# Performance work log

Measured on AMD Instinct MI355X. Metric: run time of the kernel, lower is better.

## Reference

```python
import jax, jax.numpy as jnp
import numpy as np

EPS = 1e-16


def setup_inputs() -> dict:
    key = jax.random.key(0)
    k1, k2, k3 = jax.random.split(key, 3)
    nnz, d = 2_000_000, 64
    num_cols = 50_000
    values = jax.random.normal(k1, (nnz, d), dtype=jnp.float32)
    rows = jax.random.randint(k2, (nnz,), 0, num_cols, dtype=jnp.int64)
    cols = jax.random.randint(k3, (nnz,), 0, num_cols, dtype=jnp.int64)
    indices = jnp.stack([rows, cols], axis=0)  # [2, nnz]
    return {"values": values, "indices": indices, "num_cols": num_cols}


def reference(values, indices, num_cols):
    # axis=0: pool over rows -> one pooled vector per column (segment mean),
    # then gather-broadcast back to every nonzero entry.
    seg = indices[1]  # index[1 - axis], the column index of each nnz entry
    # segment sum of values: dense [num_cols, d]
    sums = jax.ops.segment_sum(values, seg, num_segments=num_cols)
    # count of nnz per column (+ eps, matching the torch code)
    cnt = jax.ops.segment_sum(
        jnp.ones(values.shape[0], dtype=values.dtype), seg, num_segments=num_cols
    ) + EPS
    mean = sums / cnt[:, None]  # [num_cols, d]
    return mean[seg]  # [nnz, d]
```

## Files before the change

### kernel.cpp

```cpp
#include <hip/hip_runtime.h>

#define EPS 1e-16f
#define STRIDE 96

typedef float f32x4 __attribute__((ext_vector_type(4)));


__global__ void zero_cnt_kernel(int* __restrict__ ws, const int* __restrict__ nc_p) {
    const int nc = *nc_p;
    for (int i = blockIdx.x * blockDim.x + threadIdx.x; i < nc;
         i += gridDim.x * blockDim.x)
        ws[i] = 0;
}

__global__ void append_kernel(const int* __restrict__ cols, int* __restrict__ ws,
                              const int* __restrict__ nc_p, int nnz) {
    const int nc = *nc_p;
    int* cnt  = ws;
    int* perm = ws + nc;
    const int i = blockIdx.x * blockDim.x + threadIdx.x;
    if (i < nnz) {
        const int c = cols[i];
        const int r = atomicAdd(&cnt[c], 1);
        if (r < STRIDE) perm[c * STRIDE + r] = i;
    }
}

__global__ void pool_kernel(const f32x4* __restrict__ vals4,
                            int* __restrict__ ws,
                            const int* __restrict__ nc_p,
                            f32x4* __restrict__ out4) {
    const int nc = *nc_p;
    const int* cnt  = ws;
    const int* perm = ws + nc;
    const int lane = threadIdx.x & 63;
    const int g  = lane >> 4;
    const int jv = lane & 15;
    const int wave = blockIdx.x * (blockDim.x >> 6) + (threadIdx.x >> 6);
    const int nw = gridDim.x * (blockDim.x >> 6);
    for (int c = wave; c < nc; c += nw) {
        int n = cnt[c];
        if (n == 0) continue;
        n = (n > STRIDE) ? STRIDE : n;
        const int s = c * STRIDE;
        const int e = s + n;
        f32x4 acc = (f32x4)(0.f);
        for (int k = s + g; k < e; k += 4) {
            const int i = perm[k];
            const f32x4 v = __builtin_nontemporal_load(&vals4[(size_t)i * 16 + jv]);
            acc += v;
        }
        #pragma unroll
        for (int off = 16; off < 64; off <<= 1) {
            acc.x += __shfl_xor(acc.x, off);
            acc.y += __shfl_xor(acc.y, off);
            acc.z += __shfl_xor(acc.z, off);
            acc.w += __shfl_xor(acc.w, off);
        }
        const float inv = 1.0f / ((float)n + EPS);
        const f32x4 mean = acc * inv;
        for (int k = s + g; k < e; k += 4) {
            const int i = perm[k];
            __builtin_nontemporal_store(mean, &out4[(size_t)i * 16 + jv]);
        }
    }
}

extern "C" void kernel_launch(void* const* d_in, const int* in_sizes, int n_in,
                              void* d_out, int out_size, void* d_ws, size_t ws_size,
                              hipStream_t stream) {
    const float* values  = (const float*)d_in[0];
    const int*   indices = (const int*)d_in[1];
    const int*   nc_p    = (const int*)d_in[2];

    const int nnz = in_sizes[0] / 64;
    const int* cols = indices + nnz;

    int* ws = (int*)d_ws;

    const int blk = 256;
    const int grid_nnz = (nnz + blk - 1) / blk;

    zero_cnt_kernel<<<64, blk, 0, stream>>>(ws, nc_p);
    append_kernel<<<grid_nnz, blk, 0, stream>>>(cols, ws, nc_p, nnz);
    pool_kernel<<<4096, blk, 0, stream>>>((const f32x4*)values, ws, nc_p,
                                          (f32x4*)d_out);
}
```

Baseline: 409.9 us.

## Fuse zero, append and pool into one persistent kernel with grid barriers

```diff
diff --git a/kernel.cpp b/kernel.cpp
--- a/kernel.cpp
+++ b/kernel.cpp
@@ -6,38 +6,47 @@
 typedef float f32x4 __attribute__((ext_vector_type(4)));
 
 
-__global__ void zero_cnt_kernel(int* __restrict__ ws, const int* __restrict__ nc_p) {
-    const int nc = *nc_p;
-    for (int i = blockIdx.x * blockDim.x + threadIdx.x; i < nc;
-         i += gridDim.x * blockDim.x)
-        ws[i] = 0;
+__device__ __forceinline__ void gbar(int* ctr, int nblk) {
+    __syncthreads();
+    __threadfence();
+    if (threadIdx.x == 0) {
+        __hip_atomic_fetch_add(ctr, 1, __ATOMIC_ACQ_REL, __HIP_MEMORY_SCOPE_AGENT);
+        while (__hip_atomic_load(ctr, __ATOMIC_ACQUIRE, __HIP_MEMORY_SCOPE_AGENT) < nblk)
+            __builtin_amdgcn_s_sleep(4);
+    }
+    __syncthreads();
 }
 
-__global__ void append_kernel(const int* __restrict__ cols, int* __restrict__ ws,
-                              const int* __restrict__ nc_p, int nnz) {
+__global__ __launch_bounds__(256, 8)
+void fused_kernel(const f32x4* __restrict__ vals4,
+                  const int* __restrict__ cols,
+                  const int* __restrict__ nc_p,
+                  f32x4* __restrict__ out4,
+                  int* __restrict__ ws,
+                  int nnz, int nblk) {
     const int nc = *nc_p;
-    int* cnt  = ws;
-    int* perm = ws + nc;
-    const int i = blockIdx.x * blockDim.x + threadIdx.x;
-    if (i < nnz) {
+    int* bars = ws;
+    int* cnt  = ws + 16;
+    int* perm = cnt + nc;
+
+    const int tid = blockIdx.x * blockDim.x + threadIdx.x;
+    const int nth = gridDim.x * blockDim.x;
+
+    for (int i = tid; i < nc; i += nth) cnt[i] = 0;
+    gbar(&bars[0], nblk);
+
+    for (int i = tid; i < nnz; i += nth) {
         const int c = cols[i];
         const int r = atomicAdd(&cnt[c], 1);
         if (r < STRIDE) perm[c * STRIDE + r] = i;
     }
-}
+    gbar(&bars[1], nblk);
 
-__global__ void pool_kernel(const f32x4* __restrict__ vals4,
-                            int* __restrict__ ws,
-                            const int* __restrict__ nc_p,
-                            f32x4* __restrict__ out4) {
-    const int nc = *nc_p;
-    const int* cnt  = ws;
-    const int* perm = ws + nc;
     const int lane = threadIdx.x & 63;
     const int g  = lane >> 4;
     const int jv = lane & 15;
-    const int wave = blockIdx.x * (blockDim.x >> 6) + (threadIdx.x >> 6);
-    const int nw = gridDim.x * (blockDim.x >> 6);
+    const int wave = tid >> 6;
+    const int nw = nth >> 6;
     for (int c = wave; c < nc; c += nw) {
         int n = cnt[c];
         if (n == 0) continue;
@@ -69,20 +78,18 @@
 extern "C" void kernel_launch(void* const* d_in, const int* in_sizes, int n_in,
                               void* d_out, int out_size, void* d_ws, size_t ws_size,
                               hipStream_t stream) {
-    const float* values  = (const float*)d_in[0];
-    const int*   indices = (const int*)d_in[1];
-    const int*   nc_p    = (const int*)d_in[2];
+    const f32x4* vals4  = (const f32x4*)d_in[0];
+    const int* indices  = (const int*)d_in[1];
+    const int* nc_p     = (const int*)d_in[2];
 
-    const int nnz = in_sizes[0] / 64;
+    int nnz = in_sizes[0] / 64;
     const int* cols = indices + nnz;
-
+    f32x4* out4 = (f32x4*)d_out;
     int* ws = (int*)d_ws;
 
-    const int blk = 256;
-    const int grid_nnz = (nnz + blk - 1) / blk;
+    const int grid = 1024;
 
-    zero_cnt_kernel<<<64, blk, 0, stream>>>(ws, nc_p);
-    append_kernel<<<grid_nnz, blk, 0, stream>>>(cols, ws, nc_p, nnz);
-    pool_kernel<<<4096, blk, 0, stream>>>((const f32x4*)values, ws, nc_p,
-                                          (f32x4*)d_out);
+    hipMemsetAsync(d_ws, 0, 64, stream);
+
+    fused_kernel<<<grid, 256, 0, stream>>>(vals4, cols, nc_p, out4, ws, nnz, grid);
 }
```

Measured after the change: 780.5 us. 1.9x slower.
